# Kernel tuning notes

Hardware: AMD Instinct MI355X
Metric: run time of the kernel (lower is better)

## Reference

```python
import math
import jax, jax.numpy as jnp
import numpy as np

N_TOKENS = 16384
IN_FEATURES = 4096
N_EXPERTS = 64
TOP_K = 2
CAPACITY_FACTOR = 1.25
# get_capacity(n_tokens * top_k, n_experts, capacity_factor)
CAPACITY = math.ceil(N_TOKENS * TOP_K / N_EXPERTS * CAPACITY_FACTOR)  # 640


def setup_inputs() -> dict:
    key = jax.random.key(0)
    kx, kw = jax.random.split(key)
    x = jax.random.normal(kx, (N_TOKENS, IN_FEATURES), dtype=jnp.float32)
    W = jax.random.normal(kw, (N_EXPERTS, IN_FEATURES), dtype=jnp.float32) * (1.0 / math.sqrt(IN_FEATURES))
    return {"x": x, "W": W}


def reference(x, W):
    # gate: Linear(in_features, n_experts, bias=False)
    logits = jnp.einsum("nd,ed->ne", x, W)  # [N, E]
    n, e = logits.shape

    # pre_softmax=False path: topk over logits then softmax over the k scores
    scores, top_idx = jax.lax.top_k(logits, TOP_K)              # [N, K]
    probs = jax.nn.softmax(scores.astype(jnp.float32), axis=-1).astype(logits.dtype)

    rows = jnp.arange(n)[:, None]                               # [N, 1]
    # scatter probs / ones into dense [N, E] masks (topk indices per row are unique)
    top_k_masked_gates = jnp.zeros_like(logits).at[rows, top_idx].set(probs)
    top_k_mask = jnp.zeros_like(logits).at[rows, top_idx].set(1.0)

    # capacity top-k along the token dim (dim=0) -> per-expert token selection
    _, cap_idx = jax.lax.top_k(top_k_masked_gates.T, CAPACITY)  # [E, CAP] token ids
    cap_mask = jnp.zeros_like(logits).at[cap_idx, jnp.arange(e)[:, None]].set(1.0)

    # pad_to_capacity=False branch
    final_mask = jnp.logical_and(top_k_mask > 0, cap_mask > 0)  # [N, E]
    drop_mask = jnp.logical_not(final_mask)
    exceed_mask = jnp.take_along_axis(drop_mask, top_idx, axis=1)  # [N, K]
    final_probs = probs * jnp.logical_not(exceed_mask)
    final_indices = jnp.where(exceed_mask, jnp.iinfo(jnp.int32).max, top_idx)
    tokens_per_expert_before_capacity = top_k_mask.sum(0)       # [E]

    return final_probs, final_indices, tokens_per_expert_before_capacity
```

## Files before the change

### kernel.cpp

```cpp
#include <hip/hip_runtime.h>
#include <math.h>

#define N_TOK  16384
#define DIM    4096
#define NE     64
#define CAP    640
#define KC     32
#define TM     128
#define NTILES (N_TOK / TM)


__global__ __launch_bounds__(256) void gemm_logits_kernel(
    const float* __restrict__ x, const float* __restrict__ W,
    float* __restrict__ partials, int ks) {
  const int tile  = blockIdx.x % NTILES;
  const int split = blockIdx.x / NTILES;
  const int klen  = DIM / ks;
  const int k0    = split * klen;
  const int t_base = tile * TM;

  __shared__ float xT[KC][TM + 4];
  __shared__ float wT[KC][NE + 4];

  const int tid = threadIdx.x;
  const int lr = tid >> 3;
  const int lc = tid & 7;
  const int tg = tid >> 3;
  const int eg = tid & 7;

  float acc[4][8];
#pragma unroll
  for (int i = 0; i < 4; ++i)
#pragma unroll
    for (int j = 0; j < 8; ++j) acc[i][j] = 0.f;

  for (int kc = 0; kc < klen; kc += KC) {
    const int kg = k0 + kc;
#pragma unroll
    for (int i = 0; i < 4; ++i) {
      const int row = lr + i * 32;
      const float4 v = *(const float4*)(x + (size_t)(t_base + row) * DIM + kg + lc * 4);
      xT[lc * 4 + 0][row] = v.x; xT[lc * 4 + 1][row] = v.y;
      xT[lc * 4 + 2][row] = v.z; xT[lc * 4 + 3][row] = v.w;
    }
#pragma unroll
    for (int i = 0; i < 2; ++i) {
      const int row = lr + i * 32;
      const float4 v = *(const float4*)(W + (size_t)row * DIM + kg + lc * 4);
      wT[lc * 4 + 0][row] = v.x; wT[lc * 4 + 1][row] = v.y;
      wT[lc * 4 + 2][row] = v.z; wT[lc * 4 + 3][row] = v.w;
    }
    __syncthreads();
#pragma unroll
    for (int k = 0; k < KC; ++k) {
      const float4 xv = *(const float4*)&xT[k][tg * 4];
      const float4 w0 = *(const float4*)&wT[k][eg * 8];
      const float4 w1 = *(const float4*)&wT[k][eg * 8 + 4];
      const float xa[4] = {xv.x, xv.y, xv.z, xv.w};
      const float wa[8] = {w0.x, w0.y, w0.z, w0.w, w1.x, w1.y, w1.z, w1.w};
#pragma unroll
      for (int i = 0; i < 4; ++i)
#pragma unroll
        for (int j = 0; j < 8; ++j)
          acc[i][j] = fmaf(xa[i], wa[j], acc[i][j]);
    }
    __syncthreads();
  }

  float* outp = partials + (size_t)split * N_TOK * NE;
#pragma unroll
  for (int i = 0; i < 4; ++i) {
    const int t = t_base + tg * 4 + i;
    const float4 v0 = make_float4(acc[i][0], acc[i][1], acc[i][2], acc[i][3]);
    const float4 v1 = make_float4(acc[i][4], acc[i][5], acc[i][6], acc[i][7]);
    *(float4*)(outp + (size_t)t * NE + eg * 8)     = v0;
    *(float4*)(outp + (size_t)t * NE + eg * 8 + 4) = v1;
  }
}

__global__ __launch_bounds__(256) void route_kernel(
    const float* __restrict__ partials, int ks,
    float* __restrict__ out, int* __restrict__ ws_idx,
    float* __restrict__ ws_probs, int* __restrict__ counts) {
  __shared__ int cnt[NE];
  const int tid = threadIdx.x;
  if (tid < NE) cnt[tid] = 0;
  __syncthreads();
  const int t = blockIdx.x * 256 + tid;

  float b1 = -INFINITY, b2 = -INFINITY;
  int i1 = 0, i2 = 0;
  for (int e = 0; e < NE; e += 4) {
    float4 s = *(const float4*)(partials + (size_t)t * NE + e);
    for (int sp = 1; sp < ks; ++sp) {
      const float4 v = *(const float4*)(partials + (size_t)sp * N_TOK * NE + (size_t)t * NE + e);
      s.x += v.x; s.y += v.y; s.z += v.z; s.w += v.w;
    }
    const float vv[4] = {s.x, s.y, s.z, s.w};
#pragma unroll
    for (int j = 0; j < 4; ++j) {
      const float v = vv[j];
      const int idx = e + j;
      if (v > b1)      { b2 = b1; i2 = i1; b1 = v; i1 = idx; }
      else if (v > b2) { b2 = v; i2 = idx; }
    }
  }
  const float ed = expf(b2 - b1);
  const float p1 = 1.0f / (1.0f + ed);
  const float p2 = ed / (1.0f + ed);

  out[(size_t)t * 2]     = p1;
  out[(size_t)t * 2 + 1] = p2;
  out[(size_t)N_TOK * 2 + t * 2]     = (float)i1;
  out[(size_t)N_TOK * 2 + t * 2 + 1] = (float)i2;
  ws_idx[t * 2] = i1;  ws_idx[t * 2 + 1] = i2;
  ws_probs[t * 2] = p1; ws_probs[t * 2 + 1] = p2;

  atomicAdd(&cnt[i1], 1);
  atomicAdd(&cnt[i2], 1);
  __syncthreads();
  if (tid < NE) atomicAdd(&counts[tid], cnt[tid]);
}

__global__ __launch_bounds__(256) void capacity_kernel(
    const int* __restrict__ counts, const int* __restrict__ ws_idx,
    const float* __restrict__ ws_probs, float* __restrict__ out) {
  const int e = blockIdx.x;
  const int cnt = counts[e];
  if (threadIdx.x == 0) out[(size_t)N_TOK * 4 + e] = (float)cnt;
  if (cnt <= CAP) return;
  for (int i = threadIdx.x; i < N_TOK * 2; i += 256) {
    if (ws_idx[i] != e) continue;
    const float p = ws_probs[i];
    const int tok = i >> 1;
    int rank = 0;
    for (int j = 0; j < N_TOK * 2; ++j) {
      if (ws_idx[j] != e) continue;
      const float q = ws_probs[j];
      if (q > p || (q == p && (j >> 1) < tok)) ++rank;
    }
    if (rank >= CAP) {
      out[i] = 0.0f;
      out[(size_t)N_TOK * 2 + i] = 2147483648.0f;
    }
  }
}

extern "C" void kernel_launch(void* const* d_in, const int* in_sizes, int n_in,
                              void* d_out, int out_size, void* d_ws, size_t ws_size,
                              hipStream_t stream) {
  const float* x = (const float*)d_in[0];
  const float* W = (const float*)d_in[1];
  float* out = (float*)d_out;

  char* ws = (char*)d_ws;
  int*   counts   = (int*)ws;
  int*   ws_idx   = (int*)(ws + 256);
  float* ws_probs = (float*)(ws + 256 + (size_t)N_TOK * 2 * 4);
  float* partials = (float*)(ws + 262400);

  const size_t base = 262400;
  const size_t per  = (size_t)N_TOK * NE * 4;
  int ks = 1;
  if (ws_size >= base + 4 * per)      ks = 4;
  else if (ws_size >= base + 2 * per) ks = 2;

  hipMemsetAsync(counts, 0, NE * sizeof(int), stream);
  gemm_logits_kernel<<<NTILES * ks, 256, 0, stream>>>(x, W, partials, ks);
  route_kernel<<<N_TOK / 256, 256, 0, stream>>>(partials, ks, out, ws_idx, ws_probs, counts);
  capacity_kernel<<<NE, 256, 0, stream>>>(counts, ws_idx, ws_probs, out);
}
```

Before: 428.4 us.

## Restructure logits GEMM with wave-per-expert-group tiling and W read from global

Rewrites the gate GEMM so each wave owns 16 experts and each lane one token. Only the x tile is staged in LDS, using an XOR swizzle, while W is read directly from global memory (wave-uniform, so it can be cached or scalarized). It also makes the K-split a template parameter with up to 8 splits, and shrinks the route blocks to 64 threads. The goal is less LDS traffic and more parallelism for a GEMM bound by reading x. The cost is more partials traffic to write and reduce, and reliance on cache hits for W.

```diff
diff --git a/kernel.cpp b/kernel.cpp
--- a/kernel.cpp
+++ b/kernel.cpp
@@ -5,94 +5,84 @@
 #define DIM    4096
 #define NE     64
 #define CAP    640
-#define KC     32
-#define TM     128
+#define TM     64
+#define KC     64
 #define NTILES (N_TOK / TM)
 
 
-__global__ __launch_bounds__(256) void gemm_logits_kernel(
+template<int KS>
+__global__ __launch_bounds__(256, 4) void gemm_logits_kernel(
     const float* __restrict__ x, const float* __restrict__ W,
-    float* __restrict__ partials, int ks) {
-  const int tile  = blockIdx.x % NTILES;
-  const int split = blockIdx.x / NTILES;
-  const int klen  = DIM / ks;
-  const int k0    = split * klen;
+    float* __restrict__ partials) {
+  const int tile   = blockIdx.x % NTILES;
+  const int split  = blockIdx.x / NTILES;
+  const int klen   = DIM / KS;
+  const int k0     = split * klen;
   const int t_base = tile * TM;
 
-  __shared__ float xT[KC][TM + 4];
-  __shared__ float wT[KC][NE + 4];
+  __shared__ float xs[TM * KC];
 
-  const int tid = threadIdx.x;
-  const int lr = tid >> 3;
-  const int lc = tid & 7;
-  const int tg = tid >> 3;
-  const int eg = tid & 7;
+  const int tid  = threadIdx.x;
+  const int lane = tid & 63;
+  const int wave = __builtin_amdgcn_readfirstlane(tid >> 6);
+  const int e0   = wave * 16;
 
-  float acc[4][8];
+  const int s_tok = tid >> 2;
+  const int s_k4  = tid & 3;
+  const float* xrow = x + (size_t)(t_base + s_tok) * DIM + k0;
+
+  float acc[16];
 #pragma unroll
-  for (int i = 0; i < 4; ++i)
-#pragma unroll
-    for (int j = 0; j < 8; ++j) acc[i][j] = 0.f;
+  for (int i = 0; i < 16; ++i) acc[i] = 0.f;
 
   for (int kc = 0; kc < klen; kc += KC) {
-    const int kg = k0 + kc;
 #pragma unroll
     for (int i = 0; i < 4; ++i) {
-      const int row = lr + i * 32;
-      const float4 v = *(const float4*)(x + (size_t)(t_base + row) * DIM + kg + lc * 4);
-      xT[lc * 4 + 0][row] = v.x; xT[lc * 4 + 1][row] = v.y;
-      xT[lc * 4 + 2][row] = v.z; xT[lc * 4 + 3][row] = v.w;
-    }
-#pragma unroll
-    for (int i = 0; i < 2; ++i) {
-      const int row = lr + i * 32;
-      const float4 v = *(const float4*)(W + (size_t)row * DIM + kg + lc * 4);
-      wT[lc * 4 + 0][row] = v.x; wT[lc * 4 + 1][row] = v.y;
-      wT[lc * 4 + 2][row] = v.z; wT[lc * 4 + 3][row] = v.w;
+      const int k4 = s_k4 + i * 4;
+      const float4 v = *(const float4*)(xrow + kc + k4 * 4);
+      *(float4*)&xs[s_tok * KC + ((k4 ^ (s_tok & 15)) << 2)] = v;
     }
     __syncthreads();
+    const float* wbase = W + k0 + kc;
 #pragma unroll
-    for (int k = 0; k < KC; ++k) {
-      const float4 xv = *(const float4*)&xT[k][tg * 4];
-      const float4 w0 = *(const float4*)&wT[k][eg * 8];
-      const float4 w1 = *(const float4*)&wT[k][eg * 8 + 4];
-      const float xa[4] = {xv.x, xv.y, xv.z, xv.w};
-      const float wa[8] = {w0.x, w0.y, w0.z, w0.w, w1.x, w1.y, w1.z, w1.w};
+    for (int q = 0; q < 16; ++q) {
+      const float4 xv = *(const float4*)&xs[lane * KC + ((q ^ (lane & 15)) << 2)];
 #pragma unroll
-      for (int i = 0; i < 4; ++i)
-#pragma unroll
-        for (int j = 0; j < 8; ++j)
-          acc[i][j] = fmaf(xa[i], wa[j], acc[i][j]);
+      for (int e = 0; e < 16; ++e) {
+        const float4 wv = *(const float4*)(wbase + (size_t)(e0 + e) * DIM + q * 4);
+        acc[e] = fmaf(xv.x, wv.x, acc[e]);
+        acc[e] = fmaf(xv.y, wv.y, acc[e]);
+        acc[e] = fmaf(xv.z, wv.z, acc[e]);
+        acc[e] = fmaf(xv.w, wv.w, acc[e]);
+      }
     }
     __syncthreads();
   }
 
-  float* outp = partials + (size_t)split * N_TOK * NE;
+  float* outp = partials + (size_t)split * N_TOK * NE + (size_t)(t_base + lane) * NE + e0;
 #pragma unroll
-  for (int i = 0; i < 4; ++i) {
-    const int t = t_base + tg * 4 + i;
-    const float4 v0 = make_float4(acc[i][0], acc[i][1], acc[i][2], acc[i][3]);
-    const float4 v1 = make_float4(acc[i][4], acc[i][5], acc[i][6], acc[i][7]);
-    *(float4*)(outp + (size_t)t * NE + eg * 8)     = v0;
-    *(float4*)(outp + (size_t)t * NE + eg * 8 + 4) = v1;
-  }
+  for (int i = 0; i < 4; ++i)
+    *(float4*)(outp + i * 4) = make_float4(acc[i * 4], acc[i * 4 + 1], acc[i * 4 + 2], acc[i * 4 + 3]);
 }
 
-__global__ __launch_bounds__(256) void route_kernel(
-    const float* __restrict__ partials, int ks,
+template<int KS>
+__global__ __launch_bounds__(64) void route_kernel(
+    const float* __restrict__ partials,
     float* __restrict__ out, int* __restrict__ ws_idx,
     float* __restrict__ ws_probs, int* __restrict__ counts) {
   __shared__ int cnt[NE];
   const int tid = threadIdx.x;
-  if (tid < NE) cnt[tid] = 0;
+  cnt[tid] = 0;
   __syncthreads();
-  const int t = blockIdx.x * 256 + tid;
+  const int t = blockIdx.x * 64 + tid;
 
   float b1 = -INFINITY, b2 = -INFINITY;
   int i1 = 0, i2 = 0;
+#pragma unroll
   for (int e = 0; e < NE; e += 4) {
     float4 s = *(const float4*)(partials + (size_t)t * NE + e);
-    for (int sp = 1; sp < ks; ++sp) {
+#pragma unroll
+    for (int sp = 1; sp < KS; ++sp) {
       const float4 v = *(const float4*)(partials + (size_t)sp * N_TOK * NE + (size_t)t * NE + e);
       s.x += v.x; s.y += v.y; s.z += v.z; s.w += v.w;
     }
@@ -119,7 +109,7 @@
   atomicAdd(&cnt[i1], 1);
   atomicAdd(&cnt[i2], 1);
   __syncthreads();
-  if (tid < NE) atomicAdd(&counts[tid], cnt[tid]);
+  atomicAdd(&counts[tid], cnt[tid]);
 }
 
 __global__ __launch_bounds__(256) void capacity_kernel(
@@ -162,11 +152,28 @@
   const size_t base = 262400;
   const size_t per  = (size_t)N_TOK * NE * 4;
   int ks = 1;
-  if (ws_size >= base + 4 * per)      ks = 4;
+  if      (ws_size >= base + 8 * per) ks = 8;
+  else if (ws_size >= base + 4 * per) ks = 4;
   else if (ws_size >= base + 2 * per) ks = 2;
 
   hipMemsetAsync(counts, 0, NE * sizeof(int), stream);
-  gemm_logits_kernel<<<NTILES * ks, 256, 0, stream>>>(x, W, partials, ks);
-  route_kernel<<<N_TOK / 256, 256, 0, stream>>>(partials, ks, out, ws_idx, ws_probs, counts);
+  switch (ks) {
+    case 8:
+      gemm_logits_kernel<8><<<NTILES * 8, 256, 0, stream>>>(x, W, partials);
+      route_kernel<8><<<N_TOK / 64, 64, 0, stream>>>(partials, out, ws_idx, ws_probs, counts);
+      break;
+    case 4:
+      gemm_logits_kernel<4><<<NTILES * 4, 256, 0, stream>>>(x, W, partials);
+      route_kernel<4><<<N_TOK / 64, 64, 0, stream>>>(partials, out, ws_idx, ws_probs, counts);
+      break;
+    case 2:
+      gemm_logits_kernel<2><<<NTILES * 2, 256, 0, stream>>>(x, W, partials);
+      route_kernel<2><<<N_TOK / 64, 64, 0, stream>>>(partials, out, ws_idx, ws_probs, counts);
+      break;
+    default:
+      gemm_logits_kernel<1><<<NTILES * 1, 256, 0, stream>>>(x, W, partials);
+      route_kernel<1><<<N_TOK / 64, 64, 0, stream>>>(partials, out, ws_idx, ws_probs, counts);
+      break;
+  }
   capacity_kernel<<<NE, 256, 0, stream>>>(counts, ws_idx, ws_probs, out);
 }
```

Measured after the change: 734.0 us. 71.3% more time.
